# Performance work log

Hardware: AMD Instinct MI355X
Metric: run time of the kernel (lower is better)

Reference implementation:

```python
import jax, jax.numpy as jnp
import numpy as np

D_HEAD = 64


def setup_inputs() -> dict:
    key = jax.random.key(0)
    ks = jax.random.split(key, 9)
    B, S, D, H, Dh = 2, 2048, 1024, 16, D_HEAD
    scale = 0.02
    return {
        "normalized_resid_pre": jax.random.normal(ks[0], (B, S, D), jnp.float32),
        "W_Q": jax.random.normal(ks[1], (H, D, Dh), jnp.float32) * scale,
        "W_K": jax.random.normal(ks[2], (H, D, Dh), jnp.float32) * scale,
        "W_V": jax.random.normal(ks[3], (H, D, Dh), jnp.float32) * scale,
        "W_O": jax.random.normal(ks[4], (H, Dh, D), jnp.float32) * scale,
        "b_Q": jax.random.normal(ks[5], (H, Dh), jnp.float32) * scale,
        "b_K": jax.random.normal(ks[6], (H, Dh), jnp.float32) * scale,
        "b_V": jax.random.normal(ks[7], (H, Dh), jnp.float32) * scale,
        "b_O": jax.random.normal(ks[8], (D,), jnp.float32) * scale,
    }


def reference(normalized_resid_pre, W_Q, W_K, W_V, W_O, b_Q, b_K, b_V, b_O):
    x = normalized_resid_pre  # [b, s, d]
    IGNORE = jnp.float32(-1e5)
    q = jnp.einsum('bsd,hde->bshe', x, W_Q) + b_Q  # [b, s, h, dh]
    k = jnp.einsum('bsd,hde->bshe', x, W_K) + b_K
    v = jnp.einsum('bsd,hde->bshe', x, W_V) + b_V
    scores = jnp.einsum('bqhe,bkhe->bhqk', q, k) / jnp.sqrt(jnp.float32(D_HEAD))
    S = scores.shape[-1]
    causal = jnp.tril(jnp.ones((S, S), dtype=bool))  # True where allowed
    scores = jnp.where(causal, scores, IGNORE)
    pattern = jax.nn.softmax(scores, axis=-1)
    z = jnp.einsum('bkhe,bhqk->bqhe', v, pattern)
    attn_out = jnp.einsum('bqhe,hed->bqd', z, W_O) + b_O
    return attn_out
```

## Files before the change

### kernel.cpp

```cpp
#include <hip/hip_runtime.h>

typedef float f32x4 __attribute__((ext_vector_type(4)));
typedef __bf16 bf16x8_t __attribute__((ext_vector_type(8)));
typedef __bf16 bf16x4_t __attribute__((ext_vector_type(4)));
typedef unsigned int u32x2 __attribute__((ext_vector_type(2)));

#define GLOAD16(gptr, lptr)                                                        \
  __builtin_amdgcn_global_load_lds((const __attribute__((address_space(1))) void*)(gptr), \
                                   (__attribute__((address_space(3))) void*)(lptr), 16, 0, 0)

__device__ inline float fexp2(float x) {
  float r;
  asm("v_exp_f32 %0, %1" : "=v"(r) : "v"(x));
  return r;
}

union VFu { bf16x8_t v8; u32x2 w[2]; };

#define TRR(d, B, OFF) \
  asm volatile("ds_read_b64_tr_b16 %0, %1 offset:" OFF : "=v"(d) : "v"(B))

__global__ __launch_bounds__(256) void k_prep(const float* __restrict__ x,
                                              const float* __restrict__ wq,
                                              const float* __restrict__ wk,
                                              const float* __restrict__ wv,
                                              const float* __restrict__ wo,
                                              const float* __restrict__ bq,
                                              const float* __restrict__ bk,
                                              const float* __restrict__ bv,
                                              __bf16* __restrict__ xb,
                                              __bf16* __restrict__ wb1,
                                              __bf16* __restrict__ wb2,
                                              float* __restrict__ b1) {
  __shared__ __bf16 tr[64][64];
  int bid = blockIdx.x, t = threadIdx.x;
  if (bid < 4096) {
    int i = bid * 256 + t;
    float4 a = reinterpret_cast<const float4*>(x)[i];
    bf16x4_t o;
    o[0] = (__bf16)a.x; o[1] = (__bf16)a.y; o[2] = (__bf16)a.z; o[3] = (__bf16)a.w;
    reinterpret_cast<bf16x4_t*>(xb)[i] = o;
  } else if (bid < 4864) {
    int k = bid - 4096;
    int dt = k & 15, h = (k >> 4) & 15, p = k >> 8;
    const float* W = (p == 0) ? wq : (p == 1) ? wk : wv;
#pragma unroll
    for (int i = 0; i < 4; ++i) {
      int fl = i * 1024 + t * 4;
      int dd = fl >> 6, e = fl & 63;
      float4 a = *reinterpret_cast<const float4*>(W + ((size_t)(h * 1024 + dt * 64 + dd) * 64 + e));
      tr[e + 0][dd] = (__bf16)a.x; tr[e + 1][dd] = (__bf16)a.y;
      tr[e + 2][dd] = (__bf16)a.z; tr[e + 3][dd] = (__bf16)a.w;
    }
    __syncthreads();
#pragma unroll
    for (int i = 0; i < 2; ++i) {
      int ch = i * 256 + t;
      int e = ch >> 3, c8 = ch & 7;
      *reinterpret_cast<bf16x8_t*>(wb1 + ((size_t)(p * 1024 + h * 64 + e) * 1024 + dt * 64 + c8 * 8)) =
          *reinterpret_cast<const bf16x8_t*>(&tr[e][c8 * 8]);
    }
  } else if (bid < 5120) {
    int k = bid - 4864;
    int nt = k & 15, h = k >> 4;
#pragma unroll
    for (int i = 0; i < 4; ++i) {
      int fl = i * 1024 + t * 4;
      int e = fl >> 6, nn = fl & 63;
      float4 a = *reinterpret_cast<const float4*>(wo + ((size_t)(h * 64 + e) * 1024 + nt * 64 + nn));
      tr[nn + 0][e] = (__bf16)a.x; tr[nn + 1][e] = (__bf16)a.y;
      tr[nn + 2][e] = (__bf16)a.z; tr[nn + 3][e] = (__bf16)a.w;
    }
    __syncthreads();
#pragma unroll
    for (int i = 0; i < 2; ++i) {
      int ch = i * 256 + t;
      int nn = ch >> 3, c8 = ch & 7;
      *reinterpret_cast<bf16x8_t*>(wb2 + ((size_t)(nt * 64 + nn) * 1024 + h * 64 + c8 * 8)) =
          *reinterpret_cast<const bf16x8_t*>(&tr[nn][c8 * 8]);
    }
  } else {
    int n = (bid - 5120) * 256 + t;
    if (n < 3072) {
      int p = n >> 10, he = n & 1023;
      const float* s = (p == 0) ? bq : (p == 1) ? bk : bv;
      b1[n] = s[he];
    }
  }
}

template <typename OutT, int MODE, int NT>
__global__ __launch_bounds__(256) void k_gemm(const __bf16* __restrict__ A,
                                              const __bf16* __restrict__ Bt,
                                              const float* __restrict__ bias,
                                              OutT* __restrict__ C, int N, int K) {
  __shared__ __bf16 As[128 * 64];
  __shared__ __bf16 Bs[NT * 64];
  constexpr int NR = NT / 32;
  constexpr int BI = NT / 32;
  int t = threadIdx.x, l = t & 63;
  int lo = l & 15, hi = l >> 4;
  int w = t >> 6;
  int bid = blockIdx.x;
  int xcd = bid & 7, loc = bid >> 3;
  int xc = N / NT;
  int yy = loc / xc;
  int xx = loc - yy * xc;
  int m0 = (xcd * 4 + yy) * 128, n0 = xx * NT;
  int wm = (w >> 1) * 64, wn = (w & 1) * (NT / 2);
  f32x4 acc[4][NR] = {};
  for (int k0 = 0; k0 < K; k0 += 64) {
    __syncthreads();
#pragma unroll
    for (int it = 0; it < 4; ++it) {
      int idx = it * 256 + t;
      int row = idx >> 3, c = idx & 7;
      int cs = (c ^ (row & 7)) * 8;
      GLOAD16(A + (size_t)(m0 + row) * K + k0 + cs, (char*)As + (it * 256 + (t & ~63)) * 16);
    }
#pragma unroll
    for (int it = 0; it < BI; ++it) {
      int idx = it * 256 + t;
      int row = idx >> 3, c = idx & 7;
      int cs = (c ^ (row & 7)) * 8;
      GLOAD16(Bt + (size_t)(n0 + row) * K + k0 + cs, (char*)Bs + (it * 256 + (t & ~63)) * 16);
    }
    __syncthreads();
#pragma unroll
    for (int kc = 0; kc < 2; ++kc) {
      bf16x8_t af[4], bfr[NR];
#pragma unroll
      for (int mi = 0; mi < 4; ++mi) {
        int row = wm + mi * 16 + lo;
        af[mi] = *reinterpret_cast<const bf16x8_t*>(
            (char*)As + row * 128 + (((kc * 4 + hi) ^ (row & 7)) << 4));
      }
#pragma unroll
      for (int ni = 0; ni < NR; ++ni) {
        int row = wn + ni * 16 + lo;
        bfr[ni] = *reinterpret_cast<const bf16x8_t*>(
            (char*)Bs + row * 128 + (((kc * 4 + hi) ^ (row & 7)) << 4));
      }
#pragma unroll
      for (int mi = 0; mi < 4; ++mi)
#pragma unroll
        for (int ni = 0; ni < NR; ++ni)
          acc[mi][ni] = __builtin_amdgcn_mfma_f32_16x16x32_bf16(af[mi], bfr[ni], acc[mi][ni], 0, 0, 0);
    }
  }
  float qs = (MODE == 1 && n0 < 1024) ? 0.18033688f : 1.0f;
#pragma unroll
  for (int ni = 0; ni < NR; ++ni) {
    int n = n0 + wn + ni * 16 + lo;
    float bv = bias[n];
    int p = n >> 10, hh = (n >> 6) & 15, e = n & 63;
#pragma unroll
    for (int mi = 0; mi < 4; ++mi) {
#pragma unroll
      for (int r = 0; r < 4; ++r) {
        int m = m0 + wm + mi * 16 + hi * 4 + r;
        if (MODE == 0) {
          C[(size_t)m * N + n] = (OutT)(acc[mi][ni][r] + bv);
        } else {
          int b = m >> 11, sr = m & 2047;
          C[(size_t)(p * 32 + b * 16 + hh) * 131072 + sr * 64 + e] =
              (OutT)((acc[mi][ni][r] + bv) * qs);
        }
      }
    }
  }
}

__global__ __launch_bounds__(256, 4) void k_attn(const __bf16* __restrict__ QKVh,
                                                 __bf16* __restrict__ Z) {
  __shared__ __bf16 Ks[2][64 * 64];
  __shared__ __bf16 Vs[2][64 * 64];
  __shared__ __bf16 Ps[64 * 64];
  int t = threadIdx.x, l = t & 63, w = t >> 6;
  int lo = l & 15, hi = l >> 4;
  int bid = blockIdx.x;
  int xcd = bid & 7, kk = bid >> 3;
  int i = kk & 31, bhl = kk >> 5;
  int bh = xcd * 4 + bhl;
  int b = bh >> 4, h = bh & 15;
  int s16 = (w >> 1) * 64 + ((w & 1) ? (63 - i) : i);
  int qbase = s16 * 16;
  int ntW = (s16 >> 2) + 1;
  int ntH = ((127 - i) >> 2) + 1;

  const __bf16* Qbase = QKVh + (size_t)bh * 131072;
  const __bf16* Kbase = QKVh + (size_t)(32 + bh) * 131072;
  const __bf16* Vbase = QKVh + (size_t)(64 + bh) * 131072;

  int kSrc[2], vSrc[2];
#pragma unroll
  for (int it = 0; it < 2; ++it) {
    int idx = it * 256 + t;
    int row = idx >> 3, c = idx & 7;
    kSrc[it] = row * 64 + ((c ^ (row & 7)) * 8);
    int kv = ((idx >> 1) & 3) | (((idx >> 5) & 1) << 2) | (((idx >> 3) & 3) << 3) |
             (((idx >> 8) & 1) << 5);
    int e0s = ((idx & 1) << 3) | (((idx >> 6) & 3) << 4);
    vSrc[it] = kv * 64 + e0s;
  }

  bf16x8_t qf[2];
  {
    const __bf16* qptr = Qbase + (qbase + lo) * 64;
    qf[0] = *reinterpret_cast<const bf16x8_t*>(qptr + hi * 8);
    qf[1] = *reinterpret_cast<const bf16x8_t*>(qptr + 32 + hi * 8);
  }

  f32x4 zacc[4] = {};
  float lsum = 0.f;
  float mrow = -1e30f;

#define STAGE_KV(buf, tile)                                                             \
  {                                                                                     \
    GLOAD16(Kbase + (tile) * 4096 + kSrc[0], (char*)Ks[buf] + (t & ~63) * 16);          \
    GLOAD16(Kbase + (tile) * 4096 + kSrc[1], (char*)Ks[buf] + 4096 + (t & ~63) * 16);   \
    GLOAD16(Vbase + (tile) * 4096 + vSrc[0], (char*)Vs[buf] + (t & ~63) * 16);          \
    GLOAD16(Vbase + (tile) * 4096 + vSrc[1], (char*)Vs[buf] + 4096 + (t & ~63) * 16);   \
  }

  STAGE_KV(0, 0);
  __syncthreads();

  for (int tile = 0; tile < ntH; ++tile) {
    int cur = tile & 1, kv0 = tile * 64;
    bool havenext = (tile + 1 < ntH);
    if (havenext) {
      STAGE_KV(cur ^ 1, tile + 1);
      __builtin_amdgcn_sched_barrier(0);
    }
    if (tile < ntW) {
      f32x4 s[4] = {};
      __builtin_amdgcn_s_setprio(1);
#pragma unroll
      for (int cb = 0; cb < 4; ++cb) {
        int krow = cb * 16 + lo;
        const char* kp = (const char*)Ks[cur] + krow * 128;
        bf16x8_t kf0 = *reinterpret_cast<const bf16x8_t*>(kp + ((hi ^ (krow & 7)) << 4));
        bf16x8_t kf1 = *reinterpret_cast<const bf16x8_t*>(kp + (((4 + hi) ^ (krow & 7)) << 4));
        s[cb] = __builtin_amdgcn_mfma_f32_16x16x32_bf16(kf0, qf[0], s[cb], 0, 0, 0);
        s[cb] = __builtin_amdgcn_mfma_f32_16x16x32_bf16(kf1, qf[1], s[cb], 0, 0, 0);
      }
      __builtin_amdgcn_s_setprio(0);
      {
        int qabs = qbase + lo;
        if (tile == ntW - 1) {
#pragma unroll
          for (int cb = 0; cb < 4; ++cb)
#pragma unroll
            for (int r = 0; r < 4; ++r)
              if (kv0 + cb * 16 + hi * 4 + r > qabs) s[cb][r] = -1e30f;
        }
        float mt = -1e30f;
#pragma unroll
        for (int cb = 0; cb < 4; ++cb) {
          float m01 = fmaxf(s[cb][0], s[cb][1]);
          float m23 = fmaxf(s[cb][2], s[cb][3]);
          mt = fmaxf(mt, fmaxf(m01, m23));
        }
        mt = fmaxf(mt, __shfl_xor(mt, 16));
        mt = fmaxf(mt, __shfl_xor(mt, 32));
        if (!__all(mt - mrow <= 8.0f)) {
          float mnew = fmaxf(mrow, mt);
          float alpha = fexp2(mrow - mnew);
          mrow = mnew;
          lsum *= alpha;
#pragma unroll
          for (int r = 0; r < 4; ++r) {
            float at = __shfl(alpha, hi * 4 + r);
#pragma unroll
            for (int e0 = 0; e0 < 4; ++e0) zacc[e0][r] *= at;
          }
        }
        float psum = 0.f;
        int prow = w * 16 + lo;
        char* prp = (char*)Ps + prow * 128 + (hi & 1) * 8;
        int rsw = prow & 7;
#pragma unroll
        for (int cb = 0; cb < 4; ++cb) {
          bf16x4_t pp;
#pragma unroll
          for (int r = 0; r < 4; ++r) {
            float p = fexp2(s[cb][r] - mrow);
            psum += p;
            pp[r] = (__bf16)p;
          }
          *reinterpret_cast<bf16x4_t*>(prp + (((cb * 2 + (hi >> 1)) ^ rsw) << 4)) = pp;
        }
        lsum += psum;
      }
      __builtin_amdgcn_s_setprio(1);
      {
        const __attribute__((address_space(3))) char* vb =
            (const __attribute__((address_space(3))) char*)((char*)Vs[cur]) + l * 8;
        int arow = w * 16 + lo;
        {
          bf16x8_t pf = *reinterpret_cast<const bf16x8_t*>(
              (char*)Ps + arow * 128 + (((hi) ^ (arow & 7)) << 4));
          VFu u0, u1, u2, u3;
          TRR(u0.w[0], vb, "0");    TRR(u0.w[1], vb, "512");
          TRR(u1.w[0], vb, "1024"); TRR(u1.w[1], vb, "1536");
          TRR(u2.w[0], vb, "2048"); TRR(u2.w[1], vb, "2560");
          TRR(u3.w[0], vb, "3072"); TRR(u3.w[1], vb, "3584");
          asm volatile("s_waitcnt lgkmcnt(0)" ::: "memory");
          __builtin_amdgcn_sched_barrier(0);
          zacc[0] = __builtin_amdgcn_mfma_f32_16x16x32_bf16(pf, u0.v8, zacc[0], 0, 0, 0);
          zacc[1] = __builtin_amdgcn_mfma_f32_16x16x32_bf16(pf, u1.v8, zacc[1], 0, 0, 0);
          zacc[2] = __builtin_amdgcn_mfma_f32_16x16x32_bf16(pf, u2.v8, zacc[2], 0, 0, 0);
          zacc[3] = __builtin_amdgcn_mfma_f32_16x16x32_bf16(pf, u3.v8, zacc[3], 0, 0, 0);
        }
        {
          bf16x8_t pf = *reinterpret_cast<const bf16x8_t*>(
              (char*)Ps + arow * 128 + (((4 + hi) ^ (arow & 7)) << 4));
          VFu u0, u1, u2, u3;
          TRR(u0.w[0], vb, "4096"); TRR(u0.w[1], vb, "4608");
          TRR(u1.w[0], vb, "5120"); TRR(u1.w[1], vb, "5632");
          TRR(u2.w[0], vb, "6144"); TRR(u2.w[1], vb, "6656");
          TRR(u3.w[0], vb, "7168"); TRR(u3.w[1], vb, "7680");
          asm volatile("s_waitcnt lgkmcnt(0)" ::: "memory");
          __builtin_amdgcn_sched_barrier(0);
          zacc[0] = __builtin_amdgcn_mfma_f32_16x16x32_bf16(pf, u0.v8, zacc[0], 0, 0, 0);
          zacc[1] = __builtin_amdgcn_mfma_f32_16x16x32_bf16(pf, u1.v8, zacc[1], 0, 0, 0);
          zacc[2] = __builtin_amdgcn_mfma_f32_16x16x32_bf16(pf, u2.v8, zacc[2], 0, 0, 0);
          zacc[3] = __builtin_amdgcn_mfma_f32_16x16x32_bf16(pf, u3.v8, zacc[3], 0, 0, 0);
        }
      }
      __builtin_amdgcn_s_setprio(0);
    }
    __syncthreads();
  }

  float lt = lsum;
  lt += __shfl_xor(lt, 16);
  lt += __shfl_xor(lt, 32);
  float inv = 1.0f / lt;
#pragma unroll
  for (int r = 0; r < 4; ++r) {
    float lv = __shfl(inv, hi * 4 + r);
    size_t row = (size_t)(b * 2048 + qbase + hi * 4 + r);
#pragma unroll
    for (int e0 = 0; e0 < 4; ++e0)
      Z[row * 1024 + h * 64 + e0 * 16 + lo] = (__bf16)(zacc[e0][r] * lv);
  }
#undef STAGE_KV
}


extern "C" void kernel_launch(void* const* d_in, const int* in_sizes, int n_in,
                              void* d_out, int out_size, void* d_ws, size_t ws_size,
                              hipStream_t stream) {
  const float* x  = (const float*)d_in[0];
  const float* wq = (const float*)d_in[1];
  const float* wk = (const float*)d_in[2];
  const float* wv = (const float*)d_in[3];
  const float* wo = (const float*)d_in[4];
  const float* bq = (const float*)d_in[5];
  const float* bk = (const float*)d_in[6];
  const float* bv = (const float*)d_in[7];
  const float* bo = (const float*)d_in[8];
  float* out = (float*)d_out;

  char* ws = (char*)d_ws;
  __bf16* Xb   = (__bf16*)(ws);
  __bf16* WB1  = (__bf16*)(ws + 8388608);
  float*  B1   = (float*)(ws + 14680064);
  __bf16* WB2  = (__bf16*)(ws + 14692352);
  __bf16* QKVh = (__bf16*)(ws + 16789504);
  __bf16* Zb   = Xb;

  k_prep<<<5132, 256, 0, stream>>>(x, wq, wk, wv, wo, bq, bk, bv, Xb, WB1, WB2, B1);
  k_gemm<__bf16, 1, 128><<<768, 256, 0, stream>>>(Xb, WB1, B1, QKVh, 3072, 1024);
  k_attn<<<1024, 256, 0, stream>>>(QKVh, Zb);
  k_gemm<float, 0, 64><<<512, 256, 0, stream>>>(Zb, WB2, bo, out, 1024, 1024);
}
```

Before: 122.2 us.

## Parameterize GEMM M-tile and batch PV LDS reads in attention

The GEMM kernel gains an M-tile template parameter, and the output projection now uses 64x64 tiles with twice as many blocks to fill the GPU better. The block-to-row mapping now derives its per-XCD row count from the grid size. In attention, the P·V step issues all P and transposed V LDS reads up front and waits in two stages, so the first four MFMAs can start while the rest of the reads are still in flight. Smaller output GEMM tiles trade more memory traffic for more parallelism, and the issue-all-reads-first scheme raises register pressure.

```diff
diff --git a/kernel.cpp b/kernel.cpp
--- a/kernel.cpp
+++ b/kernel.cpp
@@ -89,14 +89,16 @@
   }
 }
 
-template <typename OutT, int MODE, int NT>
+template <typename OutT, int MODE, int MT, int NT>
 __global__ __launch_bounds__(256) void k_gemm(const __bf16* __restrict__ A,
                                               const __bf16* __restrict__ Bt,
                                               const float* __restrict__ bias,
                                               OutT* __restrict__ C, int N, int K) {
-  __shared__ __bf16 As[128 * 64];
+  __shared__ __bf16 As[MT * 64];
   __shared__ __bf16 Bs[NT * 64];
+  constexpr int MI = MT / 32;
   constexpr int NR = NT / 32;
+  constexpr int AI = MT / 32;
   constexpr int BI = NT / 32;
   int t = threadIdx.x, l = t & 63;
   int lo = l & 15, hi = l >> 4;
@@ -104,15 +106,16 @@
   int bid = blockIdx.x;
   int xcd = bid & 7, loc = bid >> 3;
   int xc = N / NT;
+  int rx = (int)gridDim.x / (8 * xc);
   int yy = loc / xc;
   int xx = loc - yy * xc;
-  int m0 = (xcd * 4 + yy) * 128, n0 = xx * NT;
-  int wm = (w >> 1) * 64, wn = (w & 1) * (NT / 2);
-  f32x4 acc[4][NR] = {};
+  int m0 = (xcd * rx + yy) * MT, n0 = xx * NT;
+  int wm = (w >> 1) * (MT / 2), wn = (w & 1) * (NT / 2);
+  f32x4 acc[MI][NR] = {};
   for (int k0 = 0; k0 < K; k0 += 64) {
     __syncthreads();
 #pragma unroll
-    for (int it = 0; it < 4; ++it) {
+    for (int it = 0; it < AI; ++it) {
       int idx = it * 256 + t;
       int row = idx >> 3, c = idx & 7;
       int cs = (c ^ (row & 7)) * 8;
@@ -128,9 +131,9 @@
     __syncthreads();
 #pragma unroll
     for (int kc = 0; kc < 2; ++kc) {
-      bf16x8_t af[4], bfr[NR];
-#pragma unroll
-      for (int mi = 0; mi < 4; ++mi) {
+      bf16x8_t af[MI], bfr[NR];
+#pragma unroll
+      for (int mi = 0; mi < MI; ++mi) {
         int row = wm + mi * 16 + lo;
         af[mi] = *reinterpret_cast<const bf16x8_t*>(
             (char*)As + row * 128 + (((kc * 4 + hi) ^ (row & 7)) << 4));
@@ -142,7 +145,7 @@
             (char*)Bs + row * 128 + (((kc * 4 + hi) ^ (row & 7)) << 4));
       }
 #pragma unroll
-      for (int mi = 0; mi < 4; ++mi)
+      for (int mi = 0; mi < MI; ++mi)
 #pragma unroll
         for (int ni = 0; ni < NR; ++ni)
           acc[mi][ni] = __builtin_amdgcn_mfma_f32_16x16x32_bf16(af[mi], bfr[ni], acc[mi][ni], 0, 0, 0);
@@ -155,7 +158,7 @@
     float bv = bias[n];
     int p = n >> 10, hh = (n >> 6) & 15, e = n & 63;
 #pragma unroll
-    for (int mi = 0; mi < 4; ++mi) {
+    for (int mi = 0; mi < MI; ++mi) {
 #pragma unroll
       for (int r = 0; r < 4; ++r) {
         int m = m0 + wm + mi * 16 + hi * 4 + r;
@@ -298,36 +301,35 @@
         const __attribute__((address_space(3))) char* vb =
             (const __attribute__((address_space(3))) char*)((char*)Vs[cur]) + l * 8;
         int arow = w * 16 + lo;
-        {
-          bf16x8_t pf = *reinterpret_cast<const bf16x8_t*>(
-              (char*)Ps + arow * 128 + (((hi) ^ (arow & 7)) << 4));
-          VFu u0, u1, u2, u3;
-          TRR(u0.w[0], vb, "0");    TRR(u0.w[1], vb, "512");
-          TRR(u1.w[0], vb, "1024"); TRR(u1.w[1], vb, "1536");
-          TRR(u2.w[0], vb, "2048"); TRR(u2.w[1], vb, "2560");
-          TRR(u3.w[0], vb, "3072"); TRR(u3.w[1], vb, "3584");
-          asm volatile("s_waitcnt lgkmcnt(0)" ::: "memory");
-          __builtin_amdgcn_sched_barrier(0);
-          zacc[0] = __builtin_amdgcn_mfma_f32_16x16x32_bf16(pf, u0.v8, zacc[0], 0, 0, 0);
-          zacc[1] = __builtin_amdgcn_mfma_f32_16x16x32_bf16(pf, u1.v8, zacc[1], 0, 0, 0);
-          zacc[2] = __builtin_amdgcn_mfma_f32_16x16x32_bf16(pf, u2.v8, zacc[2], 0, 0, 0);
-          zacc[3] = __builtin_amdgcn_mfma_f32_16x16x32_bf16(pf, u3.v8, zacc[3], 0, 0, 0);
-        }
-        {
-          bf16x8_t pf = *reinterpret_cast<const bf16x8_t*>(
-              (char*)Ps + arow * 128 + (((4 + hi) ^ (arow & 7)) << 4));
-          VFu u0, u1, u2, u3;
-          TRR(u0.w[0], vb, "4096"); TRR(u0.w[1], vb, "4608");
-          TRR(u1.w[0], vb, "5120"); TRR(u1.w[1], vb, "5632");
-          TRR(u2.w[0], vb, "6144"); TRR(u2.w[1], vb, "6656");
-          TRR(u3.w[0], vb, "7168"); TRR(u3.w[1], vb, "7680");
-          asm volatile("s_waitcnt lgkmcnt(0)" ::: "memory");
-          __builtin_amdgcn_sched_barrier(0);
-          zacc[0] = __builtin_amdgcn_mfma_f32_16x16x32_bf16(pf, u0.v8, zacc[0], 0, 0, 0);
-          zacc[1] = __builtin_amdgcn_mfma_f32_16x16x32_bf16(pf, u1.v8, zacc[1], 0, 0, 0);
-          zacc[2] = __builtin_amdgcn_mfma_f32_16x16x32_bf16(pf, u2.v8, zacc[2], 0, 0, 0);
-          zacc[3] = __builtin_amdgcn_mfma_f32_16x16x32_bf16(pf, u3.v8, zacc[3], 0, 0, 0);
-        }
+        char* psb = (char*)Ps + arow * 128;
+        const __attribute__((address_space(3))) char* pp0 =
+            (const __attribute__((address_space(3))) char*)(psb + ((hi ^ (arow & 7)) << 4));
+        const __attribute__((address_space(3))) char* pp1 =
+            (const __attribute__((address_space(3))) char*)(psb + (((4 + hi) ^ (arow & 7)) << 4));
+        bf16x8_t pf0, pf1;
+        asm volatile("ds_read_b128 %0, %1" : "=v"(pf0) : "v"(pp0) : "memory");
+        asm volatile("ds_read_b128 %0, %1" : "=v"(pf1) : "v"(pp1) : "memory");
+        VFu u[8];
+        TRR(u[0].w[0], vb, "0");    TRR(u[0].w[1], vb, "512");
+        TRR(u[1].w[0], vb, "1024"); TRR(u[1].w[1], vb, "1536");
+        TRR(u[2].w[0], vb, "2048"); TRR(u[2].w[1], vb, "2560");
+        TRR(u[3].w[0], vb, "3072"); TRR(u[3].w[1], vb, "3584");
+        TRR(u[4].w[0], vb, "4096"); TRR(u[4].w[1], vb, "4608");
+        TRR(u[5].w[0], vb, "5120"); TRR(u[5].w[1], vb, "5632");
+        TRR(u[6].w[0], vb, "6144"); TRR(u[6].w[1], vb, "6656");
+        TRR(u[7].w[0], vb, "7168"); TRR(u[7].w[1], vb, "7680");
+        asm volatile("s_waitcnt lgkmcnt(8)" ::: "memory");
+        __builtin_amdgcn_sched_barrier(0);
+        zacc[0] = __builtin_amdgcn_mfma_f32_16x16x32_bf16(pf0, u[0].v8, zacc[0], 0, 0, 0);
+        zacc[1] = __builtin_amdgcn_mfma_f32_16x16x32_bf16(pf0, u[1].v8, zacc[1], 0, 0, 0);
+        zacc[2] = __builtin_amdgcn_mfma_f32_16x16x32_bf16(pf0, u[2].v8, zacc[2], 0, 0, 0);
+        zacc[3] = __builtin_amdgcn_mfma_f32_16x16x32_bf16(pf0, u[3].v8, zacc[3], 0, 0, 0);
+        asm volatile("s_waitcnt lgkmcnt(0)" ::: "memory");
+        __builtin_amdgcn_sched_barrier(0);
+        zacc[0] = __builtin_amdgcn_mfma_f32_16x16x32_bf16(pf1, u[4].v8, zacc[0], 0, 0, 0);
+        zacc[1] = __builtin_amdgcn_mfma_f32_16x16x32_bf16(pf1, u[5].v8, zacc[1], 0, 0, 0);
+        zacc[2] = __builtin_amdgcn_mfma_f32_16x16x32_bf16(pf1, u[6].v8, zacc[2], 0, 0, 0);
+        zacc[3] = __builtin_amdgcn_mfma_f32_16x16x32_bf16(pf1, u[7].v8, zacc[3], 0, 0, 0);
       }
       __builtin_amdgcn_s_setprio(0);
     }
@@ -373,7 +375,7 @@
   __bf16* Zb   = Xb;
 
   k_prep<<<5132, 256, 0, stream>>>(x, wq, wk, wv, wo, bq, bk, bv, Xb, WB1, WB2, B1);
-  k_gemm<__bf16, 1, 128><<<768, 256, 0, stream>>>(Xb, WB1, B1, QKVh, 3072, 1024);
+  k_gemm<__bf16, 1, 128, 128><<<768, 256, 0, stream>>>(Xb, WB1, B1, QKVh, 3072, 1024);
   k_attn<<<1024, 256, 0, stream>>>(QKVh, Zb);
-  k_gemm<float, 0, 64><<<512, 256, 0, stream>>>(Zb, WB2, bo, out, 1024, 1024);
-}
+  k_gemm<float, 0, 64, 64><<<1024, 256, 0, stream>>>(Zb, WB2, bo, out, 1024, 1024);
+}
```

After: 120.9 us. No clear change (-1.0%).
